# Performance work log

Hardware: AMD Instinct MI355X
Metric: run time of the kernel (lower is better)

The kernel has to match this reference:

```python
import jax, jax.numpy as jnp
import numpy as np

B, L, D = 8, 3072, 256
E = 4            # num_experts
K = 2            # num_experts_per_tok
H = 4 * D        # expert mlp hidden
HS = 4 * D * 1   # shared expert hidden (n_shared_experts=1)


def setup_inputs() -> dict:
    key = jax.random.key(0)
    ks = jax.random.split(key, 16)
    s = lambda *sh: 1.0 / np.sqrt(sh[0])
    return {
        "context_c": jax.random.normal(ks[0], (B, L, D), jnp.float32),
        "time_cond": jax.random.normal(ks[1], (B, D), jnp.float32),
        "gate_w": jax.random.normal(ks[2], (3 * D, E), jnp.float32) * s(3 * D),
        "gate_b": jnp.zeros((E,), jnp.float32),
        "tmod_w": jax.random.normal(ks[3], (D, 2 * E), jnp.float32) * 0.02,
        "tmod_b": jnp.zeros((2 * E,), jnp.float32),
        "ew1": jax.random.normal(ks[4], (E, D, H), jnp.float32) * s(D),
        "eb1": jnp.zeros((E, H), jnp.float32),
        "ew2": jax.random.normal(ks[5], (E, H, D), jnp.float32) * s(H),
        "eb2": jnp.zeros((E, D), jnp.float32),
        "sw1": jax.random.normal(ks[6], (D, HS), jnp.float32) * s(D),
        "sb1": jnp.zeros((HS,), jnp.float32),
        "sw2": jax.random.normal(ks[7], (HS, D), jnp.float32) * s(HS),
        "sb2": jnp.zeros((D,), jnp.float32),
    }


def reference(context_c, time_cond, gate_w, gate_b, tmod_w, tmod_b,
              ew1, eb1, ew2, eb2, sw1, sb1, sw2, sb2):
    x = context_c
    Bc, Lc, Dc = x.shape
    Lh = Lw = Lc // 3
    Lp = Lc - Lh - Lw

    # modality aggregates for gating
    head, wrist, prop = x[:, :Lh], x[:, Lh:Lh + Lw], x[:, Lh + Lw:]
    full_agg = x.mean(axis=1)
    hp_agg = (head.sum(axis=1) + prop.sum(axis=1)) / (Lh + Lp)   # mean of cat(head, proprio)
    wp_agg = (wrist.sum(axis=1) + prop.sum(axis=1)) / (Lw + Lp)  # mean of cat(wrist, proprio)
    gate_in = jnp.concatenate([full_agg, hp_agg, wp_agg], axis=-1)  # (B, 3D)

    gate_logits = gate_in @ gate_w + gate_b  # (B, E)
    # time-conditioned modulation: SiLU -> Linear -> chunk(scale, shift)
    mod = jax.nn.silu(time_cond) @ tmod_w + tmod_b
    scale, shift = jnp.split(mod, 2, axis=-1)
    gate_logits = gate_logits * (1.0 + scale) + shift

    gate_scores = jax.nn.softmax(gate_logits, axis=-1)
    topk_w, topk_i = jax.lax.top_k(gate_scores, K)
    topk_w = topk_w / (topk_w.sum(axis=-1, keepdims=True) + 1e-8)

    # dense per-expert token-wise MLP (equivalent to the gather: MLPs act per-token)
    h = jax.nn.gelu(jnp.einsum('bld,edh->belh', x, ew1) + eb1[None, :, None, :], approximate=True)
    y = jnp.einsum('belh,ehd->beld', h, ew2) + eb2[None, :, None, :]  # (B, E, L, D)

    # modality masks: expert 0 & >=3 -> all tokens; 1 -> head+proprio; 2 -> wrist+proprio
    pos = jnp.arange(Lc)
    is_head = pos < Lh
    is_wrist = (pos >= Lh) & (pos < Lh + Lw)
    is_prop = pos >= Lh + Lw
    mask = jnp.ones((E, Lc), x.dtype)
    mask = mask.at[1].set((is_head | is_prop).astype(x.dtype))
    mask = mask.at[2].set((is_wrist | is_prop).astype(x.dtype))

    # combine weights per (batch, expert) from top-k
    w_be = (jax.nn.one_hot(topk_i, E, dtype=x.dtype) * topk_w[..., None]).sum(axis=1)  # (B, E)
    out = jnp.einsum('be,beld,el->bld', w_be, y, mask)

    # shared expert
    out = out + (jax.nn.gelu(x @ sw1 + sb1, approximate=True) @ sw2 + sb2)
    return out


if __name__ == '__main__':
    o = reference(**setup_inputs())
    print(o.shape, o.dtype)
```

## Files before the change

### kernel.cpp

```cpp
#include <hip/hip_runtime.h>
#include <stdint.h>

#define Ddim 256
#define Hdim 1024
#define LSEQ 3072

typedef __bf16 bf16x8 __attribute__((ext_vector_type(8)));
typedef unsigned short u16x8 __attribute__((ext_vector_type(8)));
typedef float f32x4 __attribute__((ext_vector_type(4)));

#define MFMA(a, b, c) __builtin_amdgcn_mfma_f32_16x16x32_bf16( \
    __builtin_bit_cast(bf16x8, (a)), __builtin_bit_cast(bf16x8, (b)), (c), 0, 0, 0)

__device__ __forceinline__ unsigned short f2bf(float f) {
  unsigned int u = __float_as_uint(f);
  u = u + 0x7FFFu + ((u >> 16) & 1u);
  return (unsigned short)(u >> 16);
}

__device__ __forceinline__ float gelu_t(float x) {
  float t = 0.7978845608028654f * (x + 0.044715f * x * x * x);
  float e = __expf(2.0f * t);
  float th = 1.0f - 2.0f / (e + 1.0f);
  return 0.5f * x * (1.0f + th);
}

__device__ __forceinline__ void glds16(const unsigned short* g, unsigned short* l) {
  __builtin_amdgcn_global_load_lds(
      (const __attribute__((address_space(1))) unsigned int*)g,
      (__attribute__((address_space(3))) unsigned int*)l, 16, 0, 0);
}

__device__ __forceinline__ void gate_eval(
    const float* __restrict__ part, const float* __restrict__ tc,
    const float* __restrict__ gw, const float* __restrict__ gb,
    const float* __restrict__ tw, const float* __restrict__ tb,
    int b, int seg, int& nm, int& wi0, int& wi1, int& wi2,
    float& sc0, float& sc1, float& sc2) {
  int lane = threadIdx.x & 63;
  float pl[4] = {0.f, 0.f, 0.f, 0.f};
  float pm[8] = {0.f, 0.f, 0.f, 0.f, 0.f, 0.f, 0.f, 0.f};
  for (int d = lane; d < 256; d += 64) {
    float Sh = 0.f, Sw = 0.f, Sp = 0.f;
    #pragma unroll
    for (int lb = 0; lb < 8; ++lb)  Sh += part[(size_t)(b * 24 + lb) * 256 + d];
    #pragma unroll
    for (int lb = 8; lb < 16; ++lb) Sw += part[(size_t)(b * 24 + lb) * 256 + d];
    #pragma unroll
    for (int lb = 16; lb < 24; ++lb) Sp += part[(size_t)(b * 24 + lb) * 256 + d];
    float vF = (Sh + Sw + Sp) * (1.0f / 3072.0f);
    float vH = (Sh + Sp) * (1.0f / 2048.0f);
    float vW = (Sw + Sp) * (1.0f / 2048.0f);
    #pragma unroll
    for (int e = 0; e < 4; ++e)
      pl[e] += vF * gw[d * 4 + e] + vH * gw[(256 + d) * 4 + e] + vW * gw[(512 + d) * 4 + e];
    float t = tc[b * 256 + d];
    float s = t / (1.0f + __expf(-t));
    #pragma unroll
    for (int j = 0; j < 8; ++j) pm[j] += s * tw[d * 8 + j];
  }
  #pragma unroll
  for (int off = 1; off < 64; off <<= 1) {
    #pragma unroll
    for (int e = 0; e < 4; ++e) pl[e] += __shfl_xor(pl[e], off);
    #pragma unroll
    for (int j = 0; j < 8; ++j) pm[j] += __shfl_xor(pm[j], off);
  }
  #pragma unroll
  for (int j = 0; j < 8; ++j) pm[j] += tb[j];
  float lg[4], sc[4];
  #pragma unroll
  for (int e = 0; e < 4; ++e) lg[e] = (pl[e] + gb[e]) * (1.0f + pm[e]) + pm[4 + e];
  float mx = fmaxf(fmaxf(lg[0], lg[1]), fmaxf(lg[2], lg[3]));
  float s = 0.0f;
  #pragma unroll
  for (int e = 0; e < 4; ++e) { sc[e] = __expf(lg[e] - mx); s += sc[e]; }
  #pragma unroll
  for (int e = 0; e < 4; ++e) sc[e] /= s;
  int i1 = 0;
  #pragma unroll
  for (int e = 1; e < 4; ++e) if (sc[e] > sc[i1]) i1 = e;
  int i2 = (i1 == 0) ? 1 : 0;
  #pragma unroll
  for (int e = 0; e < 4; ++e) if (e != i1 && sc[e] > sc[i2]) i2 = e;
  float den = sc[i1] + sc[i2] + 1e-8f;
  float w0 = 0.f, w1 = 0.f, w2v = 0.f, w3 = 0.f;
  #pragma unroll
  for (int e = 0; e < 4; ++e) {
    float v = (e == i1) ? sc[i1] / den : ((e == i2) ? sc[i2] / den : 0.0f);
    if (e == 0) w0 = v; else if (e == 1) w1 = v; else if (e == 2) w2v = v; else w3 = v;
  }
  nm = 0;
  int widx[3]; float wsc[3];
  widx[nm] = 4; wsc[nm] = 1.0f; ++nm;
  if (w0 > 0.0f) { widx[nm] = 0; wsc[nm] = w0; ++nm; }
  if (w1 > 0.0f && seg != 1) { widx[nm] = 1; wsc[nm] = w1; ++nm; }
  if (w2v > 0.0f && seg != 0) { widx[nm] = 2; wsc[nm] = w2v; ++nm; }
  if (w3 > 0.0f && nm < 3) { widx[nm] = 3; wsc[nm] = w3; ++nm; }
  wi0 = widx[0];
  wi1 = (nm > 1) ? widx[1] : widx[0];
  wi2 = (nm > 2) ? widx[2] : wi1;
  sc0 = wsc[0];
  sc1 = (nm > 1) ? wsc[1] : 0.f;
  sc2 = (nm > 2) ? wsc[2] : 0.f;
}

__global__ void k1_prep(const float* __restrict__ x, float* __restrict__ part,
                        const float* __restrict__ ew1, const float* __restrict__ sw1,
                        const float* __restrict__ ew2, const float* __restrict__ sw2,
                        unsigned short* __restrict__ wch) {
  __shared__ float tile[8448];
  int i = blockIdx.x, tid = threadIdx.x;
  if (i < 192) {
    int lb = i % 24, b = i / 24;
    const float* xg = x + ((size_t)b * LSEQ + (size_t)lb * 128) * Ddim + tid;
    float s = 0.0f;
    #pragma unroll 8
    for (int r = 0; r < 128; ++r) s += xg[(size_t)r * Ddim];
    part[(size_t)(b * 24 + lb) * 256 + tid] = s;
    return;
  }
  int pid = i - 192;
  int z = pid / 160, rem = pid % 160;
  int id = rem / 32, hc = rem % 32;
  int lane = tid & 63, lr = lane & 15, lg = lane >> 4;
  int h0 = hc * 32;
  if (z == 0) {
    const float* src = (id < 4) ? (ew1 + (size_t)id * Ddim * Hdim) : sw1;
    #pragma unroll
    for (int p = 0; p < 8; ++p) {
      int row = p * 32 + (tid >> 3);
      int c = (tid & 7) * 4;
      float4 v = *(const float4*)&src[(size_t)row * Hdim + h0 + c];
      tile[row * 33 + c] = v.x; tile[row * 33 + c + 1] = v.y;
      tile[row * 33 + c + 2] = v.z; tile[row * 33 + c + 3] = v.w;
    }
    __syncthreads();
    unsigned short* dst = wch + ((size_t)(id * 32 + hc)) * 16384;
    #pragma unroll
    for (int p = 0; p < 4; ++p) {
      int f = tid + p * 256;
      int hg = (f >> 6) & 1, k = f >> 7;
      u16x8 r;
      #pragma unroll
      for (int j = 0; j < 8; ++j) r[j] = f2bf(tile[(k * 32 + lg * 8 + j) * 33 + hg * 16 + lr]);
      *(u16x8*)&dst[(size_t)f * 8] = r;
    }
  } else {
    const float* src = (id < 4) ? (ew2 + (size_t)id * Hdim * Ddim) : sw2;
    #pragma unroll
    for (int p = 0; p < 8; ++p) {
      int hh = p * 4 + (tid >> 6);
      int c = (tid & 63) * 4;
      float4 v = *(const float4*)&src[(size_t)(h0 + hh) * Ddim + c];
      int ci = c + (c >> 5);
      tile[hh * 264 + ci] = v.x; tile[hh * 264 + ci + 1] = v.y;
      tile[hh * 264 + ci + 2] = v.z; tile[hh * 264 + ci + 3] = v.w;
    }
    __syncthreads();
    unsigned short* dst = wch + ((size_t)(id * 32 + hc)) * 16384 + 8192;
    #pragma unroll
    for (int p = 0; p < 4; ++p) {
      int f = tid + p * 256;
      int dg = f >> 6;
      u16x8 r;
      #pragma unroll
      for (int j = 0; j < 8; ++j) {
        int c = dg * 16 + lr;
        r[j] = f2bf(tile[(lg * 8 + j) * 264 + c + (c >> 5)]);
      }
      *(u16x8*)&dst[(size_t)f * 8] = r;
    }
  }
}

__global__ __launch_bounds__(256, 2) void moe_main(
    const float* __restrict__ x, const unsigned short* __restrict__ wch,
    const float* __restrict__ eb1, const float* __restrict__ sb1,
    const float* __restrict__ eb2, const float* __restrict__ sb2,
    const float* __restrict__ part, const float* __restrict__ tc,
    const float* __restrict__ gw, const float* __restrict__ gb,
    const float* __restrict__ tw, const float* __restrict__ tb,
    unsigned short* __restrict__ kpart, float* __restrict__ out) {
  __shared__ __align__(16) unsigned short lds[3 * 8192 + 64 * 40];
  unsigned short* const hid = lds + 3 * 8192;

  const int i = blockIdx.x;
  const int b = i & 7, q = (i >> 3) & 1, t = i >> 4;
  const int tid = threadIdx.x;
  const int wave = tid >> 6, lane = tid & 63;
  const int lr = lane & 15, lg = lane >> 4;
  const int wm = wave >> 1, wn = wave & 1;
  const int seg = t >> 4;

  int nm, wi0, wi1, wi2;
  float sc0, sc1, sc2;
  gate_eval(part, tc, gw, gb, tw, tb, b, seg, nm, wi0, wi1, wi2, sc0, sc1, sc2);
  const int total = nm * 16;

  u16x8 xf[8][2];
  const float* xb = x + ((size_t)(b * LSEQ + t * 64 + wm * 32 + lr)) * Ddim;
  #pragma unroll
  for (int k = 0; k < 8; ++k) {
    #pragma unroll
    for (int mf = 0; mf < 2; ++mf) {
      const float* p = xb + (size_t)(mf * 16) * Ddim + k * 32 + lg * 8;
      float4 v0 = *(const float4*)p;
      float4 v1 = *(const float4*)(p + 4);
      u16x8 r;
      r[0] = f2bf(v0.x); r[1] = f2bf(v0.y); r[2] = f2bf(v0.z); r[3] = f2bf(v0.w);
      r[4] = f2bf(v1.x); r[5] = f2bf(v1.y); r[6] = f2bf(v1.z); r[7] = f2bf(v1.w);
      xf[k][mf] = r;
    }
  }

  f32x4 oacc[4][4];
  const f32x4 fz = {0.f, 0.f, 0.f, 0.f};
  #pragma unroll
  for (int mf = 0; mf < 4; ++mf)
    #pragma unroll
    for (int nf = 0; nf < 4; ++nf) oacc[mf][nf] = fz;

  unsigned short* p0 = lds;
  unsigned short* p1 = lds + 8192;
  unsigned short* p2 = lds + 16384;

  {
    const unsigned short* c0 = wch + (size_t)(wi0 * 32 + q * 16) * 16384;
    #pragma unroll
    for (int qq = 0; qq < 4; ++qq) glds16(c0 + tid * 8 + qq * 2048, p0 + tid * 8 + qq * 2048);
    int j1 = (total > 1) ? 1 : 0;
    int id1 = (j1 >> 4) == 0 ? wi0 : wi1;
    const unsigned short* c1 = wch + (size_t)(id1 * 32 + q * 16 + (j1 & 15)) * 16384;
    #pragma unroll
    for (int qq = 0; qq < 4; ++qq) glds16(c1 + tid * 8 + qq * 2048, p1 + tid * 8 + qq * 2048);
  }
  asm volatile("s_waitcnt vmcnt(4)" ::: "memory");
  __builtin_amdgcn_s_barrier();
  __builtin_amdgcn_sched_barrier(0);

  for (int j = 0; j < total; ++j) {
    const int m = j >> 4, hc = q * 16 + (j & 15);
    const int id = (m == 0) ? wi0 : ((m == 1) ? wi1 : wi2);
    const float wscale = (m == 0) ? sc0 : ((m == 1) ? sc1 : sc2);
    const unsigned short* cb = wch + (size_t)(id * 32 + hc) * 16384;

    const float* b1g = (id < 4) ? (eb1 + id * Hdim) : sb1;
    float b1v = b1g[hc * 32 + wn * 16 + lr];
    u16x8 wbU[4];
    const unsigned short* w2c = cb + 8192 + ((size_t)(wave * 4) * 64 + lane) * 8;
    #pragma unroll
    for (int nf = 0; nf < 4; ++nf) wbU[nf] = *(const u16x8*)(w2c + nf * 512);
    __builtin_amdgcn_sched_barrier(0);

    {
      int j2 = (j + 2 < total) ? j + 2 : total - 1;
      int m2 = j2 >> 4;
      int id2 = (m2 == 0) ? wi0 : ((m2 == 1) ? wi1 : wi2);
      const unsigned short* cb2 = wch + (size_t)(id2 * 32 + q * 16 + (j2 & 15)) * 16384;
      #pragma unroll
      for (int qq = 0; qq < 4; ++qq)
        glds16(cb2 + tid * 8 + qq * 2048, p2 + tid * 8 + qq * 2048);
    }
    __builtin_amdgcn_sched_barrier(0);

    asm volatile("s_waitcnt vmcnt(18)" ::: "memory");
    __builtin_amdgcn_sched_barrier(0);

    f32x4 a1[2];
    a1[0] = fz; a1[1] = fz;
    __builtin_amdgcn_s_setprio(1);
    #pragma unroll
    for (int k = 0; k < 8; ++k) {
      u16x8 bf = *(const u16x8*)&p0[((k * 2 + wn) * 64 + lane) * 8];
      a1[0] = MFMA(xf[k][0], bf, a1[0]);
      a1[1] = MFMA(xf[k][1], bf, a1[1]);
    }
    __builtin_amdgcn_s_setprio(0);
    #pragma unroll
    for (int mr = 0; mr < 2; ++mr)
      #pragma unroll
      for (int r = 0; r < 4; ++r)
        hid[(wm * 32 + mr * 16 + lg * 4 + r) * 40 + wn * 16 + lr] =
            f2bf(gelu_t(a1[mr][r] + b1v) * wscale);
    asm volatile("s_waitcnt lgkmcnt(0)" ::: "memory");
    __builtin_amdgcn_s_barrier();
    __builtin_amdgcn_sched_barrier(0);

    u16x8 ha[4];
    #pragma unroll
    for (int mf = 0; mf < 4; ++mf)
      ha[mf] = *(const u16x8*)&hid[(mf * 16 + lr) * 40 + lg * 8];
    __builtin_amdgcn_s_setprio(1);
    #pragma unroll
    for (int mf = 0; mf < 4; ++mf)
      #pragma unroll
      for (int nf = 0; nf < 4; ++nf)
        oacc[mf][nf] = MFMA(ha[mf], wbU[nf], oacc[mf][nf]);
    __builtin_amdgcn_s_setprio(0);
    __builtin_amdgcn_s_barrier();
    __builtin_amdgcn_sched_barrier(0);

    unsigned short* tmp = p0; p0 = p1; p1 = p2; p2 = tmp;
  }

  if (q == 0) {
    float* og = out + ((size_t)b * LSEQ + t * 64) * Ddim;
    #pragma unroll
    for (int nf = 0; nf < 4; ++nf) {
      int dcol = wave * 64 + nf * 16 + lr;
      float bias = sb2[dcol];
      if (wi0 < 4) bias += sc0 * eb2[wi0 * Ddim + dcol];
      if (nm > 1 && wi1 < 4) bias += sc1 * eb2[wi1 * Ddim + dcol];
      if (nm > 2 && wi2 < 4) bias += sc2 * eb2[wi2 * Ddim + dcol];
      #pragma unroll
      for (int mf = 0; mf < 4; ++mf)
        #pragma unroll
        for (int r = 0; r < 4; ++r)
          og[(size_t)(mf * 16 + lg * 4 + r) * Ddim + dcol] = oacc[mf][nf][r] + bias;
    }
  } else {
    unsigned short* pg = kpart + ((size_t)b * LSEQ + t * 64) * Ddim;
    #pragma unroll
    for (int nf = 0; nf < 4; ++nf) {
      int dcol = wave * 64 + nf * 16 + lr;
      #pragma unroll
      for (int mf = 0; mf < 4; ++mf)
        #pragma unroll
        for (int r = 0; r < 4; ++r)
          pg[(size_t)(mf * 16 + lg * 4 + r) * Ddim + dcol] = f2bf(oacc[mf][nf][r]);
    }
  }
}

__global__ void combine(const unsigned short* __restrict__ kpart, float* __restrict__ out) {
  size_t base = ((size_t)blockIdx.x * 256 + threadIdx.x) * 8;
  u16x8 p = *(const u16x8*)&kpart[base];
  float4 o0 = *(const float4*)&out[base];
  float4 o1 = *(const float4*)&out[base + 4];
  o0.x += __uint_as_float((unsigned)p[0] << 16);
  o0.y += __uint_as_float((unsigned)p[1] << 16);
  o0.z += __uint_as_float((unsigned)p[2] << 16);
  o0.w += __uint_as_float((unsigned)p[3] << 16);
  o1.x += __uint_as_float((unsigned)p[4] << 16);
  o1.y += __uint_as_float((unsigned)p[5] << 16);
  o1.z += __uint_as_float((unsigned)p[6] << 16);
  o1.w += __uint_as_float((unsigned)p[7] << 16);
  *(float4*)&out[base] = o0;
  *(float4*)&out[base + 4] = o1;
}


extern "C" void kernel_launch(void* const* d_in, const int* in_sizes, int n_in,
                              void* d_out, int out_size, void* d_ws, size_t ws_size,
                              hipStream_t stream) {
  const float* x      = (const float*)d_in[0];
  const float* tc     = (const float*)d_in[1];
  const float* gate_w = (const float*)d_in[2];
  const float* gate_b = (const float*)d_in[3];
  const float* tmod_w = (const float*)d_in[4];
  const float* tmod_b = (const float*)d_in[5];
  const float* ew1    = (const float*)d_in[6];
  const float* eb1    = (const float*)d_in[7];
  const float* ew2    = (const float*)d_in[8];
  const float* eb2    = (const float*)d_in[9];
  const float* sw1    = (const float*)d_in[10];
  const float* sb1    = (const float*)d_in[11];
  const float* sw2    = (const float*)d_in[12];
  const float* sb2    = (const float*)d_in[13];
  float* out = (float*)d_out;

  char* wsb = (char*)d_ws;
  float* ws_part = (float*)wsb;
  unsigned short* wch = (unsigned short*)(wsb + 196608);
  unsigned short* kpart = (unsigned short*)(wsb + 196608 + 10485760);

  k1_prep<<<512, 256, 0, stream>>>(x, ws_part, ew1, sw1, ew2, sw2, wch);
  moe_main<<<768, 256, 0, stream>>>(x, wch, eb1, sb1, eb2, sb2, ws_part, tc,
                                    gate_w, gate_b, tmod_w, tmod_b, kpart, out);
  combine<<<3072, 256, 0, stream>>>(kpart, out);
}
```

Baseline: 270.2 us.

## Drop hidden-dim split across blocks, removing bf16 partials and combine kernel

Each block now processes all 32 hidden chunks for its 64-token tile instead of splitting them across two blocks, so the bf16 partial-output buffer and the separate combine kernel go away. The first GEMM is reorganised with weights as the A operand and each wave owning 16 tokens. W2 fragments and biases are prefetched one chunk ahead via a two-way unrolled loop. GELU is rewritten as a sigmoid form using exp2 and rcp intrinsics. The trade-off is that the grid halves to 384 blocks, which may leave the GPU underfilled, and each block's serial loop becomes twice as long.

```diff
diff --git a/kernel.cpp b/kernel.cpp
--- a/kernel.cpp
+++ b/kernel.cpp
@@ -16,13 +16,6 @@
   unsigned int u = __float_as_uint(f);
   u = u + 0x7FFFu + ((u >> 16) & 1u);
   return (unsigned short)(u >> 16);
-}
-
-__device__ __forceinline__ float gelu_t(float x) {
-  float t = 0.7978845608028654f * (x + 0.044715f * x * x * x);
-  float e = __expf(2.0f * t);
-  float th = 1.0f - 2.0f / (e + 1.0f);
-  return 0.5f * x * (1.0f + th);
 }
 
 __device__ __forceinline__ void glds16(const unsigned short* g, unsigned short* l) {
@@ -181,37 +174,36 @@
     const float* __restrict__ part, const float* __restrict__ tc,
     const float* __restrict__ gw, const float* __restrict__ gb,
     const float* __restrict__ tw, const float* __restrict__ tb,
-    unsigned short* __restrict__ kpart, float* __restrict__ out) {
-  __shared__ __align__(16) unsigned short lds[3 * 8192 + 64 * 40];
+    float* __restrict__ out) {
+  __shared__ __align__(16) unsigned short lds[3 * 8192 + 64 * 44];
   unsigned short* const hid = lds + 3 * 8192;
 
   const int i = blockIdx.x;
-  const int b = i & 7, q = (i >> 3) & 1, t = i >> 4;
+  const int b = i & 7, t = i >> 3;
   const int tid = threadIdx.x;
   const int wave = tid >> 6, lane = tid & 63;
   const int lr = lane & 15, lg = lane >> 4;
-  const int wm = wave >> 1, wn = wave & 1;
   const int seg = t >> 4;
 
   int nm, wi0, wi1, wi2;
   float sc0, sc1, sc2;
   gate_eval(part, tc, gw, gb, tw, tb, b, seg, nm, wi0, wi1, wi2, sc0, sc1, sc2);
-  const int total = nm * 16;
-
-  u16x8 xf[8][2];
-  const float* xb = x + ((size_t)(b * LSEQ + t * 64 + wm * 32 + lr)) * Ddim;
+  const int total = nm * 32;
+
+#define CHUNK_ID(JJ) ((((JJ) >> 5) == 0) ? wi0 : ((((JJ) >> 5) == 1) ? wi1 : wi2))
+#define CHUNK_PTR(JJ) (wch + (size_t)(CHUNK_ID(JJ) * 32 + ((JJ) & 31)) * 16384)
+
+  u16x8 xf[8];
+  const float* xb = x + ((size_t)(b * LSEQ + t * 64 + wave * 16 + lr)) * Ddim;
   #pragma unroll
   for (int k = 0; k < 8; ++k) {
-    #pragma unroll
-    for (int mf = 0; mf < 2; ++mf) {
-      const float* p = xb + (size_t)(mf * 16) * Ddim + k * 32 + lg * 8;
-      float4 v0 = *(const float4*)p;
-      float4 v1 = *(const float4*)(p + 4);
-      u16x8 r;
-      r[0] = f2bf(v0.x); r[1] = f2bf(v0.y); r[2] = f2bf(v0.z); r[3] = f2bf(v0.w);
-      r[4] = f2bf(v1.x); r[5] = f2bf(v1.y); r[6] = f2bf(v1.z); r[7] = f2bf(v1.w);
-      xf[k][mf] = r;
-    }
+    const float* p = xb + k * 32 + lg * 8;
+    float4 v0 = *(const float4*)p;
+    float4 v1 = *(const float4*)(p + 4);
+    u16x8 r;
+    r[0] = f2bf(v0.x); r[1] = f2bf(v0.y); r[2] = f2bf(v0.z); r[3] = f2bf(v0.w);
+    r[4] = f2bf(v1.x); r[5] = f2bf(v1.y); r[6] = f2bf(v1.z); r[7] = f2bf(v1.w);
+    xf[k] = r;
   }
 
   f32x4 oacc[4][4];
@@ -221,133 +213,126 @@
     #pragma unroll
     for (int nf = 0; nf < 4; ++nf) oacc[mf][nf] = fz;
 
-  unsigned short* p0 = lds;
-  unsigned short* p1 = lds + 8192;
-  unsigned short* p2 = lds + 16384;
+  unsigned short* c0 = lds;
+  unsigned short* c1 = lds + 8192;
+  unsigned short* c2 = lds + 16384;
+
+  float4 b1A[2], b1B[2];
+  u16x8 wbA[4], wbB[4];
 
   {
-    const unsigned short* c0 = wch + (size_t)(wi0 * 32 + q * 16) * 16384;
-    #pragma unroll
-    for (int qq = 0; qq < 4; ++qq) glds16(c0 + tid * 8 + qq * 2048, p0 + tid * 8 + qq * 2048);
-    int j1 = (total > 1) ? 1 : 0;
-    int id1 = (j1 >> 4) == 0 ? wi0 : wi1;
-    const unsigned short* c1 = wch + (size_t)(id1 * 32 + q * 16 + (j1 & 15)) * 16384;
-    #pragma unroll
-    for (int qq = 0; qq < 4; ++qq) glds16(c1 + tid * 8 + qq * 2048, p1 + tid * 8 + qq * 2048);
-  }
-  asm volatile("s_waitcnt vmcnt(4)" ::: "memory");
+    const unsigned short* cb0 = CHUNK_PTR(0);
+    #pragma unroll
+    for (int qq = 0; qq < 4; ++qq) glds16(cb0 + tid * 8 + qq * 2048, c0 + tid * 8 + qq * 2048);
+    const int j1 = (total > 1) ? 1 : 0;
+    const unsigned short* cb1 = CHUNK_PTR(j1);
+    #pragma unroll
+    for (int qq = 0; qq < 4; ++qq) glds16(cb1 + tid * 8 + qq * 2048, c1 + tid * 8 + qq * 2048);
+    const float* b1g0 = (wi0 < 4) ? (eb1 + wi0 * Hdim) : sb1;
+    b1A[0] = *(const float4*)&b1g0[lg * 4];
+    b1A[1] = *(const float4*)&b1g0[16 + lg * 4];
+    const unsigned short* w20 = cb0 + 8192 + ((size_t)((wave * 4) * 64 + lane)) * 8;
+    #pragma unroll
+    for (int nf = 0; nf < 4; ++nf) wbA[nf] = *(const u16x8*)(w20 + nf * 512);
+  }
+  asm volatile("s_waitcnt vmcnt(10)" ::: "memory");
   __builtin_amdgcn_s_barrier();
   __builtin_amdgcn_sched_barrier(0);
 
-  for (int j = 0; j < total; ++j) {
-    const int m = j >> 4, hc = q * 16 + (j & 15);
-    const int id = (m == 0) ? wi0 : ((m == 1) ? wi1 : wi2);
-    const float wscale = (m == 0) ? sc0 : ((m == 1) ? sc1 : sc2);
-    const unsigned short* cb = wch + (size_t)(id * 32 + hc) * 16384;
-
-    const float* b1g = (id < 4) ? (eb1 + id * Hdim) : sb1;
-    float b1v = b1g[hc * 32 + wn * 16 + lr];
-    u16x8 wbU[4];
-    const unsigned short* w2c = cb + 8192 + ((size_t)(wave * 4) * 64 + lane) * 8;
-    #pragma unroll
-    for (int nf = 0; nf < 4; ++nf) wbU[nf] = *(const u16x8*)(w2c + nf * 512);
-    __builtin_amdgcn_sched_barrier(0);
-
-    {
-      int j2 = (j + 2 < total) ? j + 2 : total - 1;
-      int m2 = j2 >> 4;
-      int id2 = (m2 == 0) ? wi0 : ((m2 == 1) ? wi1 : wi2);
-      const unsigned short* cb2 = wch + (size_t)(id2 * 32 + q * 16 + (j2 & 15)) * 16384;
-      #pragma unroll
-      for (int qq = 0; qq < 4; ++qq)
-        glds16(cb2 + tid * 8 + qq * 2048, p2 + tid * 8 + qq * 2048);
-    }
-    __builtin_amdgcn_sched_barrier(0);
-
-    asm volatile("s_waitcnt vmcnt(18)" ::: "memory");
-    __builtin_amdgcn_sched_barrier(0);
-
-    f32x4 a1[2];
-    a1[0] = fz; a1[1] = fz;
-    __builtin_amdgcn_s_setprio(1);
-    #pragma unroll
-    for (int k = 0; k < 8; ++k) {
-      u16x8 bf = *(const u16x8*)&p0[((k * 2 + wn) * 64 + lane) * 8];
-      a1[0] = MFMA(xf[k][0], bf, a1[0]);
-      a1[1] = MFMA(xf[k][1], bf, a1[1]);
-    }
-    __builtin_amdgcn_s_setprio(0);
-    #pragma unroll
-    for (int mr = 0; mr < 2; ++mr)
+#define ITER(J, CUR, NXT2, B1U, WBU, B1P, WBP)                                   \
+  {                                                                              \
+       \
+    const int jn = ((J) + 1 < total) ? (J) + 1 : total - 1;                      \
+    const unsigned short* cbn = CHUNK_PTR(jn);                                   \
+    const int idn = CHUNK_ID(jn);                                                \
+    const float* b1gn = (idn < 4) ? (eb1 + idn * Hdim) : sb1;                    \
+    (B1P)[0] = *(const float4*)&b1gn[(jn & 31) * 32 + lg * 4];                   \
+    (B1P)[1] = *(const float4*)&b1gn[(jn & 31) * 32 + 16 + lg * 4];              \
+    const unsigned short* w2n = cbn + 8192 + ((size_t)((wave * 4) * 64 + lane)) * 8; \
+    _Pragma("unroll")                                                            \
+    for (int nf = 0; nf < 4; ++nf) (WBP)[nf] = *(const u16x8*)(w2n + nf * 512);  \
+    __builtin_amdgcn_sched_barrier(0);                                           \
+                                                              \
+    {                                                                            \
+      const int j2 = ((J) + 2 < total) ? (J) + 2 : total - 1;                    \
+      const unsigned short* cb2 = CHUNK_PTR(j2);                                 \
+      _Pragma("unroll")                                                          \
+      for (int qq = 0; qq < 4; ++qq)                                             \
+        glds16(cb2 + tid * 8 + qq * 2048, (NXT2) + tid * 8 + qq * 2048);         \
+    }                                                                            \
+    __builtin_amdgcn_sched_barrier(0);                                           \
+                         \
+    asm volatile("s_waitcnt vmcnt(20)" ::: "memory");                            \
+    __builtin_amdgcn_sched_barrier(0);                                           \
+                                           \
+    f32x4 a1[2]; a1[0] = fz; a1[1] = fz;                                         \
+    __builtin_amdgcn_s_setprio(1);                                               \
+    _Pragma("unroll")                                                            \
+    for (int k = 0; k < 8; ++k) {                                                \
+      u16x8 w0 = *(const u16x8*)&(CUR)[((k * 2 + 0) * 64 + lane) * 8];           \
+      u16x8 w1 = *(const u16x8*)&(CUR)[((k * 2 + 1) * 64 + lane) * 8];           \
+      a1[0] = MFMA(w0, xf[k], a1[0]);                                            \
+      a1[1] = MFMA(w1, xf[k], a1[1]);                                            \
+    }                                                                            \
+    __builtin_amdgcn_s_setprio(0);                                               \
+                     \
+    const float wsc_ = (((J) >> 5) == 0) ? sc0 : ((((J) >> 5) == 1) ? sc1 : sc2);\
+    _Pragma("unroll")                                                            \
+    for (int hg = 0; hg < 2; ++hg) {                                             \
+      ushort4 st;                                                                \
+      _Pragma("unroll")                                                          \
+      for (int r = 0; r < 4; ++r) {                                              \
+        float z = a1[hg][r] + (B1U)[hg][r];                                      \
+        float u = z * z;                                                         \
+        float tp = z * __builtin_fmaf(u, -0.1029434f, -2.3022117f);              \
+        float e = __builtin_amdgcn_exp2f(tp);                                    \
+        float rr = __builtin_amdgcn_rcpf(e + 1.0f);                              \
+        st[r] = f2bf(z * wsc_ * rr);                                             \
+      }                                                                          \
+      *(ushort4*)&hid[(wave * 16 + lr) * 44 + hg * 16 + lg * 4] = st;            \
+    }                                                                            \
+    asm volatile("s_waitcnt lgkmcnt(0)" ::: "memory");                           \
+    __builtin_amdgcn_s_barrier();                                                \
+    __builtin_amdgcn_sched_barrier(0);                                           \
+                                         \
+    u16x8 ha[4];                                                                 \
+    _Pragma("unroll")                                                            \
+    for (int mf = 0; mf < 4; ++mf)                                               \
+      ha[mf] = *(const u16x8*)&hid[(mf * 16 + lr) * 44 + lg * 8];                \
+    __builtin_amdgcn_s_setprio(1);                                               \
+    _Pragma("unroll")                                                            \
+    for (int mf = 0; mf < 4; ++mf)                                               \
+      _Pragma("unroll")                                                          \
+      for (int nf = 0; nf < 4; ++nf)                                             \
+        oacc[mf][nf] = MFMA(ha[mf], (WBU)[nf], oacc[mf][nf]);                    \
+    __builtin_amdgcn_s_setprio(0);                                               \
+    __builtin_amdgcn_s_barrier();                                                \
+    __builtin_amdgcn_sched_barrier(0);                                           \
+  }
+
+  for (int j = 0; j < total; j += 2) {
+    ITER(j,     c0, c2, b1A, wbA, b1B, wbB);
+    ITER(j + 1, c1, c0, b1B, wbB, b1A, wbA);
+    unsigned short* tmp = c0; c0 = c2; c2 = c1; c1 = tmp;
+  }
+#undef ITER
+#undef CHUNK_PTR
+#undef CHUNK_ID
+
+  float* og = out + ((size_t)b * LSEQ + t * 64) * Ddim;
+  #pragma unroll
+  for (int nf = 0; nf < 4; ++nf) {
+    int dcol = wave * 64 + nf * 16 + lr;
+    float bias = sb2[dcol];
+    if (wi0 < 4) bias += sc0 * eb2[wi0 * Ddim + dcol];
+    if (nm > 1 && wi1 < 4) bias += sc1 * eb2[wi1 * Ddim + dcol];
+    if (nm > 2 && wi2 < 4) bias += sc2 * eb2[wi2 * Ddim + dcol];
+    #pragma unroll
+    for (int mf = 0; mf < 4; ++mf)
       #pragma unroll
       for (int r = 0; r < 4; ++r)
-        hid[(wm * 32 + mr * 16 + lg * 4 + r) * 40 + wn * 16 + lr] =
-            f2bf(gelu_t(a1[mr][r] + b1v) * wscale);
-    asm volatile("s_waitcnt lgkmcnt(0)" ::: "memory");
-    __builtin_amdgcn_s_barrier();
-    __builtin_amdgcn_sched_barrier(0);
-
-    u16x8 ha[4];
-    #pragma unroll
-    for (int mf = 0; mf < 4; ++mf)
-      ha[mf] = *(const u16x8*)&hid[(mf * 16 + lr) * 40 + lg * 8];
-    __builtin_amdgcn_s_setprio(1);
-    #pragma unroll
-    for (int mf = 0; mf < 4; ++mf)
-      #pragma unroll
-      for (int nf = 0; nf < 4; ++nf)
-        oacc[mf][nf] = MFMA(ha[mf], wbU[nf], oacc[mf][nf]);
-    __builtin_amdgcn_s_setprio(0);
-    __builtin_amdgcn_s_barrier();
-    __builtin_amdgcn_sched_barrier(0);
-
-    unsigned short* tmp = p0; p0 = p1; p1 = p2; p2 = tmp;
-  }
-
-  if (q == 0) {
-    float* og = out + ((size_t)b * LSEQ + t * 64) * Ddim;
-    #pragma unroll
-    for (int nf = 0; nf < 4; ++nf) {
-      int dcol = wave * 64 + nf * 16 + lr;
-      float bias = sb2[dcol];
-      if (wi0 < 4) bias += sc0 * eb2[wi0 * Ddim + dcol];
-      if (nm > 1 && wi1 < 4) bias += sc1 * eb2[wi1 * Ddim + dcol];
-      if (nm > 2 && wi2 < 4) bias += sc2 * eb2[wi2 * Ddim + dcol];
-      #pragma unroll
-      for (int mf = 0; mf < 4; ++mf)
-        #pragma unroll
-        for (int r = 0; r < 4; ++r)
-          og[(size_t)(mf * 16 + lg * 4 + r) * Ddim + dcol] = oacc[mf][nf][r] + bias;
-    }
-  } else {
-    unsigned short* pg = kpart + ((size_t)b * LSEQ + t * 64) * Ddim;
-    #pragma unroll
-    for (int nf = 0; nf < 4; ++nf) {
-      int dcol = wave * 64 + nf * 16 + lr;
-      #pragma unroll
-      for (int mf = 0; mf < 4; ++mf)
-        #pragma unroll
-        for (int r = 0; r < 4; ++r)
-          pg[(size_t)(mf * 16 + lg * 4 + r) * Ddim + dcol] = f2bf(oacc[mf][nf][r]);
-    }
-  }
-}
-
-__global__ void combine(const unsigned short* __restrict__ kpart, float* __restrict__ out) {
-  size_t base = ((size_t)blockIdx.x * 256 + threadIdx.x) * 8;
-  u16x8 p = *(const u16x8*)&kpart[base];
-  float4 o0 = *(const float4*)&out[base];
-  float4 o1 = *(const float4*)&out[base + 4];
-  o0.x += __uint_as_float((unsigned)p[0] << 16);
-  o0.y += __uint_as_float((unsigned)p[1] << 16);
-  o0.z += __uint_as_float((unsigned)p[2] << 16);
-  o0.w += __uint_as_float((unsigned)p[3] << 16);
-  o1.x += __uint_as_float((unsigned)p[4] << 16);
-  o1.y += __uint_as_float((unsigned)p[5] << 16);
-  o1.z += __uint_as_float((unsigned)p[6] << 16);
-  o1.w += __uint_as_float((unsigned)p[7] << 16);
-  *(float4*)&out[base] = o0;
-  *(float4*)&out[base + 4] = o1;
+        og[(size_t)(mf * 16 + lg * 4 + r) * Ddim + dcol] = oacc[mf][nf][r] + bias;
+  }
 }
 
 
@@ -373,10 +358,8 @@
   char* wsb = (char*)d_ws;
   float* ws_part = (float*)wsb;
   unsigned short* wch = (unsigned short*)(wsb + 196608);
-  unsigned short* kpart = (unsigned short*)(wsb + 196608 + 10485760);
 
   k1_prep<<<512, 256, 0, stream>>>(x, ws_part, ew1, sw1, ew2, sw2, wch);
-  moe_main<<<768, 256, 0, stream>>>(x, wch, eb1, sb1, eb2, sb2, ws_part, tc,
-                                    gate_w, gate_b, tmod_w, tmod_b, kpart, out);
-  combine<<<3072, 256, 0, stream>>>(kpart, out);
-}
+  moe_main<<<384, 256, 0, stream>>>(x, wch, eb1, sb1, eb2, sb2, ws_part, tc,
+                                    gate_w, gate_b, tmod_w, tmod_b, out);
+}
```

Result: no change. 266.7 us (-1.3%).
